# Performance work log

Hardware: AMD Instinct MI355X
Metric: run time of the kernel (lower is better)

The kernel has to match this reference:

```python
import jax, jax.numpy as jnp
import numpy as np

B, L = 256, 8192
DIM, NPAT, HIST, WIN = 256, 64, 32, 8


def setup_inputs() -> dict:
    key = jax.random.key(0)
    ks = jax.random.split(key, 6)
    return {
        "x": jax.random.normal(ks[0], (B, L), dtype=jnp.float32),
        "avg_init": jax.random.normal(ks[1], (B, NPAT), dtype=jnp.float32),
        "conv_w": jax.random.normal(ks[2], (DIM, 1, HIST), dtype=jnp.float32) * 0.1,
        "conv_b": jax.random.normal(ks[3], (DIM,), dtype=jnp.float32) * 0.1,
        "keys_w": jax.random.normal(ks[4], (NPAT, DIM), dtype=jnp.float32) * 0.1,
        "shapes_w": jax.random.normal(ks[5], (WIN, NPAT), dtype=jnp.float32) * 0.1,
    }


def reference(x, avg_init, conv_w, conv_b, keys_w, shapes_w):
    b, l = x.shape
    n_pat = keys_w.shape[0]
    hist = conv_w.shape[2]
    win = shapes_w.shape[0]

    # randn avg_scores, centered (module draws fresh randn each forward; we take it as input)
    avg0 = avg_init - jnp.mean(avg_init, axis=-1, keepdims=True)

    padded = jnp.pad(x, ((0, 0), (hist - 1, 0)))[:, None, :]  # [B,1,L+hist-1]
    out = jax.lax.conv_general_dilated(
        padded, conv_w, window_strides=(win,), padding="VALID",
        dimension_numbers=("NCH", "OIH", "NCH"))
    out = out + conv_b[None, :, None]                     # [B,dim,T]
    out = jnp.transpose(out, (2, 0, 1))                   # [T,B,dim]

    # relu6(keys(out)) -> attn scores [T,B,n_pat]
    scores = jnp.clip(jnp.einsum("tbd,pd->tbp", out, keys_w), 0.0, 6.0)

    # sequential balanced-routing scan over T with running average scores
    def step(avg, score):                                 # avg,score: [B,n_pat]
        idx = jnp.argmax(score - avg, axis=-1)
        prob = jax.nn.one_hot(idx, n_pat, dtype=score.dtype)
        return avg + prob - 1.0 / n_pat, prob

    _, probs = jax.lax.scan(step, avg0, scores)           # probs: [T,B,n_pat]
    probs = jnp.transpose(probs, (1, 0, 2))               # [B,T,n_pat]

    signal = jnp.einsum("btp,wp->btw", probs, shapes_w).reshape(b, -1)[:, :l]
    return jax.nn.relu(signal - x)
```

## Files before the change

kernel.cpp:

```cpp
#include <hip/hip_runtime.h>


constexpr int Bb = 256, Ll = 8192, DIMc = 256, NPAT = 64, HIST = 32, WINc = 8;
constexpr int Tt = Ll / WINc;
constexpr int TC = 32;
constexpr int NC = Tt / TC;
constexpr float CINV = 1.0f / 64.0f;

#define DPP_STAGE(m, ctrl, rmask)                                              \
  (m) = fmaxf((m), __int_as_float(__builtin_amdgcn_update_dpp(                 \
            __float_as_int(m), __float_as_int(m), (ctrl), (rmask), 0xF, false)))

__global__ __launch_bounds__(256) void precompute_kernel(
    const float* __restrict__ conv_w, const float* __restrict__ conv_b,
    const float* __restrict__ keys_w, float* __restrict__ wsf) {
  __shared__ float part[8][32];
  __shared__ float bred[4];
  const int p = blockIdx.x;
  const int t = threadIdx.x;
  const int h = t & 31, g = t >> 5;
  const float* kwp = keys_w + (size_t)p * DIMc;

  float acc = 0.f;
#pragma unroll
  for (int dd = 0; dd < 32; ++dd) {
    int d = g * 32 + dd;
    acc = fmaf(kwp[d], conv_w[d * HIST + h], acc);
  }
  part[g][h] = acc;

  float bp = kwp[t] * conv_b[t];
#pragma unroll
  for (int off = 32; off; off >>= 1) bp += __shfl_down(bp, off);
  if ((t & 63) == 0) bred[t >> 6] = bp;
  __syncthreads();

  if (t < 32) {
    float s = 0.f;
#pragma unroll
    for (int gg = 0; gg < 8; ++gg) s += part[gg][t];
    wsf[(t >> 2) * (NPAT * 4) + p * 4 + (t & 3)] = s;
  } else if (t == 32) {
    wsf[NPAT * HIST + p] = (bred[0] + bred[1]) + (bred[2] + bred[3]);
  }
}

__global__ __launch_bounds__(256) void shaper_kernel(
    const float* __restrict__ x, const float* __restrict__ avg_init,
    const float* __restrict__ shapes_w, const float* __restrict__ wsf,
    float* __restrict__ out) {
  __shared__ __align__(16) float xpad[HIST - 1 + Ll + 1];
  __shared__ float scb[2][TC * NPAT];
  __shared__ int   idxb[Tt];
  __shared__ float shp[WINc * NPAT];

  const int b    = blockIdx.x;
  const int tid  = threadIdx.x;
  const int wid  = tid >> 6;
  const int lane = tid & 63;
  const float* xrow = x + (size_t)b * Ll;

  if (tid < HIST - 1) xpad[tid] = 0.f;
  {
    const float4* xv4 = (const float4*)xrow;
#pragma unroll
    for (int k = 0; k < 8; ++k) {
      int i4 = k * 256 + tid;
      float4 v = xv4[i4];
      float* dst = xpad + HIST - 1 + i4 * 4;
      dst[0] = v.x; dst[1] = v.y; dst[2] = v.z; dst[3] = v.w;
    }
  }
  for (int i = tid; i < WINc * NPAT; i += 256) shp[i] = shapes_w[i];

  float4 w2v[8];
  float  b2 = 0.f;
  if (wid > 0) {
    const float4* w2g = (const float4*)wsf;
#pragma unroll
    for (int h4 = 0; h4 < 8; ++h4) w2v[h4] = w2g[h4 * 64 + lane];
    b2 = wsf[NPAT * HIST + lane];
  }
  float av = 0.f;
  if (wid == 0) {
    const float* ai = avg_init + (size_t)b * NPAT;
    float s = 0.f;
    for (int j = 0; j < NPAT; ++j) s += ai[j];
    av = ai[lane] - s * (1.0f / NPAT);
  }
  __syncthreads();

  auto fill = [&](int c, float* __restrict__ sb) {
    int base = c * TC;
    for (int tl = wid - 1; tl < TC; tl += 3) {
      int t = base + tl;
      const float4* xw = (const float4*)(xpad + t * WINc);
      float acc = b2;
#pragma unroll
      for (int h4 = 0; h4 < 8; ++h4) {
        float4 xv = xw[h4];
        float4 wv = w2v[h4];
        acc = fmaf(xv.x, wv.x, acc);
        acc = fmaf(xv.y, wv.y, acc);
        acc = fmaf(xv.z, wv.z, acc);
        acc = fmaf(xv.w, wv.w, acc);
      }
      sb[tl * NPAT + lane] = fminf(fmaxf(acc, 0.f), 6.f);
    }
  };

  auto scan_chunk = [&](const float* __restrict__ sb, int tbase) {
    float r[TC];
#pragma unroll
    for (int i = 0; i < TC; ++i) r[i] = sb[i * NPAT + lane];
    float v = r[0] - av;
    int stash = 0;
#pragma unroll
    for (int i = 0; i < TC; ++i) {
      float t0 = av - CINV;
      float t1 = (av + 1.0f) - CINV;
      float vA = 0.f, vB = 0.f;
      if (i + 1 < TC) { vA = r[i + 1] - t0; vB = r[i + 1] - t1; }
      float m = v;
      DPP_STAGE(m, 0xB1, 0xF);
      DPP_STAGE(m, 0x4E, 0xF);
      DPP_STAGE(m, 0x141, 0xF);
      DPP_STAGE(m, 0x140, 0xF);
      DPP_STAGE(m, 0x142, 0xA);
      DPP_STAGE(m, 0x143, 0xC);
      float gmax = __int_as_float(
          __builtin_amdgcn_readlane(__float_as_int(m), 63));
      bool e = (v == gmax);
      av = e ? t1 : t0;
      if (i + 1 < TC) v = e ? vB : vA;
      unsigned long long mk = __ballot(e);
      int winner = __ffsll(mk) - 1;
      stash = (lane == i) ? winner : stash;
    }
    if (lane < TC) idxb[tbase + lane] = stash;
  };

  if (wid > 0) fill(0, scb[0]);
  __syncthreads();

  for (int c = 0; c < NC; ++c) {
    if (wid == 0) {
      scan_chunk(scb[c & 1], c * TC);
    } else if (c + 1 < NC) {
      fill(c + 1, scb[(c + 1) & 1]);
    }
    __syncthreads();
  }

  float4* outv = (float4*)(out + (size_t)b * Ll);
#pragma unroll
  for (int k = 0; k < 8; ++k) {
    int i4 = k * 256 + tid;
    int l0 = i4 * 4;
    int t  = l0 >> 3;
    int w0 = l0 & 7;
    int p  = idxb[t];
    float4 o;
    o.x = fmaxf(shp[(w0 + 0) * NPAT + p] - xpad[HIST - 1 + l0 + 0], 0.f);
    o.y = fmaxf(shp[(w0 + 1) * NPAT + p] - xpad[HIST - 1 + l0 + 1], 0.f);
    o.z = fmaxf(shp[(w0 + 2) * NPAT + p] - xpad[HIST - 1 + l0 + 2], 0.f);
    o.w = fmaxf(shp[(w0 + 3) * NPAT + p] - xpad[HIST - 1 + l0 + 3], 0.f);
    outv[i4] = o;
  }
}

extern "C" void kernel_launch(void* const* d_in, const int* in_sizes, int n_in,
                              void* d_out, int out_size, void* d_ws, size_t ws_size,
                              hipStream_t stream) {
  const float* x        = (const float*)d_in[0];
  const float* avg_init = (const float*)d_in[1];
  const float* conv_w   = (const float*)d_in[2];
  const float* conv_b   = (const float*)d_in[3];
  const float* keys_w   = (const float*)d_in[4];
  const float* shapes_w = (const float*)d_in[5];
  float* wsf = (float*)d_ws;

  precompute_kernel<<<NPAT, 256, 0, stream>>>(conv_w, conv_b, keys_w, wsf);
  shaper_kernel<<<Bb, 256, 0, stream>>>(x, avg_init, shapes_w, wsf,
                                        (float*)d_out);
}
```

Measured before the change: 175.5 us.

## Reformulate routing scan as count-offset scores and resolve two steps per reduction

Folds the running-average bookkeeping into precomputed scores: the fill stage stores score minus initial average plus t/64, so the scan only has to track an integer win count per lane. The scan then handles two timesteps per iteration, doing a plain max reduction for the even step and a top-2 reduction for the odd step in parallel. The odd step's winner is derived from the top-2 and ballots, so the two DPP chains no longer wait on each other and the sequential dependency per step shrinks. Initial average centering now uses a DPP sum instead of a serial 64-element loop. The trade-off is more ballots and DPP ops per iteration, plus a risk of floating-point ordering differences: t*CINV accumulated in a different order may change argmax ties relative to the reference.

```diff
diff --git a/kernel.cpp b/kernel.cpp
--- a/kernel.cpp
+++ b/kernel.cpp
@@ -1,4 +1,5 @@
 #include <hip/hip_runtime.h>
+#include <math.h>
 
 
 constexpr int Bb = 256, Ll = 8192, DIMc = 256, NPAT = 64, HIST = 32, WINc = 8;
@@ -10,6 +11,24 @@
 #define DPP_STAGE(m, ctrl, rmask)                                              \
   (m) = fmaxf((m), __int_as_float(__builtin_amdgcn_update_dpp(                 \
             __float_as_int(m), __float_as_int(m), (ctrl), (rmask), 0xF, false)))
+
+#define TOP2_STAGE(M, S, ctrl, rmask)                                          \
+  do {                                                                         \
+    float _Md = __int_as_float(__builtin_amdgcn_update_dpp(                    \
+        __float_as_int(M), __float_as_int(M), (ctrl), (rmask), 0xF, false));   \
+    float _Sd = __int_as_float(__builtin_amdgcn_update_dpp(                    \
+        __float_as_int(S), __float_as_int(S), (ctrl), (rmask), 0xF, false));   \
+    float _mn = fminf((M), _Md);                                               \
+    (M) = fmaxf((M), _Md);                                                     \
+    (S) = fmaxf(fmaxf((S), _Sd), _mn);                                         \
+  } while (0)
+
+#define DPP_ADDF(s, ctrl, rmask)                                               \
+  do {                                                                         \
+    int _si = __float_as_int(s);                                               \
+    int _ti = __builtin_amdgcn_update_dpp(_si, _si, (ctrl), (rmask), 0xF, false); \
+    (s) += __int_as_float(_ti);                                                \
+  } while (0)
 
 __global__ __launch_bounds__(256) void precompute_kernel(
     const float* __restrict__ conv_w, const float* __restrict__ conv_b,
@@ -73,6 +92,20 @@
   }
   for (int i = tid; i < WINc * NPAT; i += 256) shp[i] = shapes_w[i];
 
+  float av0;
+  {
+    float s = avg_init[(size_t)b * NPAT + lane];
+    float t = s;
+    DPP_ADDF(t, 0xB1, 0xF);
+    DPP_ADDF(t, 0x4E, 0xF);
+    DPP_ADDF(t, 0x141, 0xF);
+    DPP_ADDF(t, 0x140, 0xF);
+    DPP_ADDF(t, 0x142, 0xA);
+    DPP_ADDF(t, 0x143, 0xC);
+    float tot = __int_as_float(__builtin_amdgcn_readlane(__float_as_int(t), 63));
+    av0 = s - tot * CINV;
+  }
+
   float4 w2v[8];
   float  b2 = 0.f;
   if (wid > 0) {
@@ -80,13 +113,6 @@
 #pragma unroll
     for (int h4 = 0; h4 < 8; ++h4) w2v[h4] = w2g[h4 * 64 + lane];
     b2 = wsf[NPAT * HIST + lane];
-  }
-  float av = 0.f;
-  if (wid == 0) {
-    const float* ai = avg_init + (size_t)b * NPAT;
-    float s = 0.f;
-    for (int j = 0; j < NPAT; ++j) s += ai[j];
-    av = ai[lane] - s * (1.0f / NPAT);
   }
   __syncthreads();
 
@@ -105,37 +131,58 @@
         acc = fmaf(xv.z, wv.z, acc);
         acc = fmaf(xv.w, wv.w, acc);
       }
-      sb[tl * NPAT + lane] = fminf(fmaxf(acc, 0.f), 6.f);
+      float sc = fminf(fmaxf(acc, 0.f), 6.f);
+      sb[tl * NPAT + lane] = (sc - av0) + (float)t * CINV;
     }
   };
+
+  float cnt = 0.f;
+  int   swA = 64, swB = 64;
 
   auto scan_chunk = [&](const float* __restrict__ sb, int tbase) {
     float r[TC];
 #pragma unroll
     for (int i = 0; i < TC; ++i) r[i] = sb[i * NPAT + lane];
-    float v = r[0] - av;
     int stash = 0;
 #pragma unroll
-    for (int i = 0; i < TC; ++i) {
-      float t0 = av - CINV;
-      float t1 = (av + 1.0f) - CINV;
-      float vA = 0.f, vB = 0.f;
-      if (i + 1 < TC) { vA = r[i + 1] - t0; vB = r[i + 1] - t1; }
-      float m = v;
-      DPP_STAGE(m, 0xB1, 0xF);
-      DPP_STAGE(m, 0x4E, 0xF);
-      DPP_STAGE(m, 0x141, 0xF);
-      DPP_STAGE(m, 0x140, 0xF);
-      DPP_STAGE(m, 0x142, 0xA);
-      DPP_STAGE(m, 0x143, 0xC);
-      float gmax = __int_as_float(
-          __builtin_amdgcn_readlane(__float_as_int(m), 63));
-      bool e = (v == gmax);
-      av = e ? t1 : t0;
-      if (i + 1 < TC) v = e ? vB : vA;
-      unsigned long long mk = __ballot(e);
-      int winner = __ffsll(mk) - 1;
-      stash = (lane == i) ? winner : stash;
+    for (int k = 0; k < TC / 2; ++k) {
+      cnt += (lane == swA) ? 1.0f : 0.0f;
+      cnt += (lane == swB) ? 1.0f : 0.0f;
+      float zE = r[2 * k]     - cnt;
+      float zO = r[2 * k + 1] - cnt;
+      float mE = zE;
+      DPP_STAGE(mE, 0xB1, 0xF);
+      DPP_STAGE(mE, 0x4E, 0xF);
+      DPP_STAGE(mE, 0x141, 0xF);
+      DPP_STAGE(mE, 0x140, 0xF);
+      DPP_STAGE(mE, 0x142, 0xA);
+      DPP_STAGE(mE, 0x143, 0xC);
+      float M = zO, S = -INFINITY;
+      TOP2_STAGE(M, S, 0xB1, 0xF);
+      TOP2_STAGE(M, S, 0x4E, 0xF);
+      TOP2_STAGE(M, S, 0x141, 0xF);
+      TOP2_STAGE(M, S, 0x140, 0xF);
+      TOP2_STAGE(M, S, 0x142, 0xA);
+      TOP2_STAGE(M, S, 0x143, 0xC);
+      float sME = __int_as_float(__builtin_amdgcn_readlane(__float_as_int(mE), 63));
+      float sMO = __int_as_float(__builtin_amdgcn_readlane(__float_as_int(M), 63));
+      float sSO = __int_as_float(__builtin_amdgcn_readlane(__float_as_int(S), 63));
+      unsigned long long E1E = __ballot(zE == sME);
+      int wA = __ffsll(E1E) - 1;
+      unsigned long long E1O = __ballot(zO == sMO);
+      unsigned long long ES  = __ballot(zO == sSO);
+      float zO1 = zO - 1.0f;
+      unsigned long long GT = __ballot(zO1 > sSO);
+      unsigned long long GE = __ballot(zO1 >= sSO);
+      int jO = __ffsll(E1O) - 1;
+      int jS = __ffsll(ES) - 1;
+      int gt = (int)((GT >> wA) & 1);
+      int ge = (int)((GE >> wA) & 1);
+      int mn = wA < jS ? wA : jS;
+      int wB = (jO != wA) ? jO : (gt ? wA : (ge ? mn : jS));
+      stash = (lane == 2 * k)     ? wA : stash;
+      stash = (lane == 2 * k + 1) ? wB : stash;
+      swA = wA; swB = wB;
     }
     if (lane < TC) idxb[tbase + lane] = stash;
   };
```

Result: slower. 212.7 us (+21.2%).

## Fold running-average offset into scores to shorten the serial scan loop

Applied to the files above, without the earlier changes.

Rewrites the scan recurrence so the fill warps emit score - avg0 + t/64, leaving the serial scan warp to track only a per-lane integer-like counter C. Each step then needs one fewer add on the dependent chain. Winner indices are packed into 64-bit words held in uniform registers instead of a per-lane stash, and the avg_init centering now uses a DPP reduction instead of a 64-iteration serial loop. The reformulation changes floating-point rounding (t/64 grows large), so argmax ties or near-ties could resolve differently from the reference.

```diff
diff --git a/kernel.cpp b/kernel.cpp
--- a/kernel.cpp
+++ b/kernel.cpp
@@ -10,6 +10,13 @@
 #define DPP_STAGE(m, ctrl, rmask)                                              \
   (m) = fmaxf((m), __int_as_float(__builtin_amdgcn_update_dpp(                 \
             __float_as_int(m), __float_as_int(m), (ctrl), (rmask), 0xF, false)))
+
+#define DPP_ADDF(s, ctrl, rmask)                                               \
+  do {                                                                         \
+    int _si = __float_as_int(s);                                               \
+    int _ti = __builtin_amdgcn_update_dpp(_si, _si, (ctrl), (rmask), 0xF, false); \
+    (s) += __int_as_float(_ti);                                                \
+  } while (0)
 
 __global__ __launch_bounds__(256) void precompute_kernel(
     const float* __restrict__ conv_w, const float* __restrict__ conv_b,
@@ -51,7 +58,7 @@
     float* __restrict__ out) {
   __shared__ __align__(16) float xpad[HIST - 1 + Ll + 1];
   __shared__ float scb[2][TC * NPAT];
-  __shared__ int   idxb[Tt];
+  __shared__ unsigned long long idxp[NC * 4];
   __shared__ float shp[WINc * NPAT];
 
   const int b    = blockIdx.x;
@@ -73,6 +80,20 @@
   }
   for (int i = tid; i < WINc * NPAT; i += 256) shp[i] = shapes_w[i];
 
+  float av0;
+  {
+    float s = avg_init[(size_t)b * NPAT + lane];
+    float t = s;
+    DPP_ADDF(t, 0xB1, 0xF);
+    DPP_ADDF(t, 0x4E, 0xF);
+    DPP_ADDF(t, 0x141, 0xF);
+    DPP_ADDF(t, 0x140, 0xF);
+    DPP_ADDF(t, 0x142, 0xA);
+    DPP_ADDF(t, 0x143, 0xC);
+    float tot = __int_as_float(__builtin_amdgcn_readlane(__float_as_int(t), 63));
+    av0 = s - tot * CINV;
+  }
+
   float4 w2v[8];
   float  b2 = 0.f;
   if (wid > 0) {
@@ -80,13 +101,6 @@
 #pragma unroll
     for (int h4 = 0; h4 < 8; ++h4) w2v[h4] = w2g[h4 * 64 + lane];
     b2 = wsf[NPAT * HIST + lane];
-  }
-  float av = 0.f;
-  if (wid == 0) {
-    const float* ai = avg_init + (size_t)b * NPAT;
-    float s = 0.f;
-    for (int j = 0; j < NPAT; ++j) s += ai[j];
-    av = ai[lane] - s * (1.0f / NPAT);
   }
   __syncthreads();
 
@@ -105,22 +119,23 @@
         acc = fmaf(xv.z, wv.z, acc);
         acc = fmaf(xv.w, wv.w, acc);
       }
-      sb[tl * NPAT + lane] = fminf(fmaxf(acc, 0.f), 6.f);
+      float sc = fminf(fmaxf(acc, 0.f), 6.f);
+      sb[tl * NPAT + lane] = (sc - av0) + (float)t * CINV;
     }
   };
 
-  auto scan_chunk = [&](const float* __restrict__ sb, int tbase) {
-    float r[TC];
-#pragma unroll
-    for (int i = 0; i < TC; ++i) r[i] = sb[i * NPAT + lane];
-    float v = r[0] - av;
-    int stash = 0;
+  float C = 0.f;
+
+  auto scan_chunk = [&](const float* __restrict__ sb, int cidx) {
+    float U[TC];
+#pragma unroll
+    for (int i = 0; i < TC; ++i) U[i] = sb[i * NPAT + lane];
+    unsigned long long pk0 = 0, pk1 = 0, pk2 = 0, pk3 = 0;
+    float v = U[0] - C;
 #pragma unroll
     for (int i = 0; i < TC; ++i) {
-      float t0 = av - CINV;
-      float t1 = (av + 1.0f) - CINV;
       float vA = 0.f, vB = 0.f;
-      if (i + 1 < TC) { vA = r[i + 1] - t0; vB = r[i + 1] - t1; }
+      if (i + 1 < TC) { vA = U[i + 1] - C; vB = vA - 1.0f; }
       float m = v;
       DPP_STAGE(m, 0xB1, 0xF);
       DPP_STAGE(m, 0x4E, 0xF);
@@ -131,13 +146,22 @@
       float gmax = __int_as_float(
           __builtin_amdgcn_readlane(__float_as_int(m), 63));
       bool e = (v == gmax);
-      av = e ? t1 : t0;
+      float C1 = C + 1.0f;
+      unsigned long long mk = __ballot(e);
+      unsigned long long w = (unsigned long long)(__ffsll(mk) - 1);
+      if (i < 8)       pk0 |= w << (8 * (i & 7));
+      else if (i < 16) pk1 |= w << (8 * (i & 7));
+      else if (i < 24) pk2 |= w << (8 * (i & 7));
+      else             pk3 |= w << (8 * (i & 7));
+      C = e ? C1 : C;
       if (i + 1 < TC) v = e ? vB : vA;
-      unsigned long long mk = __ballot(e);
-      int winner = __ffsll(mk) - 1;
-      stash = (lane == i) ? winner : stash;
-    }
-    if (lane < TC) idxb[tbase + lane] = stash;
+    }
+    if (lane == 0) {
+      idxp[cidx * 4 + 0] = pk0;
+      idxp[cidx * 4 + 1] = pk1;
+      idxp[cidx * 4 + 2] = pk2;
+      idxp[cidx * 4 + 3] = pk3;
+    }
   };
 
   if (wid > 0) fill(0, scb[0]);
@@ -145,7 +169,7 @@
 
   for (int c = 0; c < NC; ++c) {
     if (wid == 0) {
-      scan_chunk(scb[c & 1], c * TC);
+      scan_chunk(scb[c & 1], c);
     } else if (c + 1 < NC) {
       fill(c + 1, scb[(c + 1) & 1]);
     }
@@ -159,7 +183,7 @@
     int l0 = i4 * 4;
     int t  = l0 >> 3;
     int w0 = l0 & 7;
-    int p  = idxb[t];
+    int p  = (int)((idxp[t >> 3] >> (8 * (t & 7))) & 63ull);
     float4 o;
     o.x = fmaxf(shp[(w0 + 0) * NPAT + p] - xpad[HIST - 1 + l0 + 0], 0.f);
     o.y = fmaxf(shp[(w0 + 1) * NPAT + p] - xpad[HIST - 1 + l0 + 1], 0.f);
```

New measurement: 170.3 us, median of 2. 3.0% less time.
